# Performance work log

Hardware: AMD Instinct MI355X
Metric: run time of the kernel (lower is better)

Reference implementation:

```python
import jax, jax.numpy as jnp
import numpy as np

A = 4096      # alleles
RPA = 20      # mean reads per allele
R = A * RPA   # total reads per data source
C = 12        # input channels (pileup features)
L = 32        # read window length
D = 32        # hidden feature dim
NOUT = 2


def setup_inputs() -> dict:
    key = jax.random.key(0)
    k = jax.random.split(key, 8)
    # ragged read counts per allele (alternating 16/24, mean 20, sums to R)
    counts0 = np.tile(np.array([16, 24], dtype=np.int64), A // 2)
    counts1 = np.tile(np.array([24, 16], dtype=np.int64), A // 2)
    return {
        "tensors0": jax.random.normal(k[0], (R, C, L), dtype=jnp.float32),
        "tensors1": jax.random.normal(k[1], (R, C, L), dtype=jnp.float32),
        "W0": jax.random.normal(k[2], (D, C), dtype=jnp.float32) * 0.1,
        "b0": jnp.zeros((D,), dtype=jnp.float32),
        "W1": jax.random.normal(k[3], (D, C), dtype=jnp.float32) * 0.1,
        "b1": jnp.zeros((D,), dtype=jnp.float32),
        "W2": jax.random.normal(k[4], (NOUT, 2 * D), dtype=jnp.float32) * 0.1,
        "b2": jnp.zeros((NOUT,), dtype=jnp.float32),
        "numReadsPerAllele0": jnp.asarray(counts0),
        "numReadsPerAllele1": jnp.asarray(counts1),
        "numAllelesPerSite": jnp.full((A // 2,), 2, dtype=jnp.int64),
        "depthMultiplier0": jnp.asarray(counts0, dtype=jnp.float32),
        "depthMultiplier1": jnp.asarray(counts1, dtype=jnp.float32),
    }


def _frames(t, W, b):
    # pointwise read-feature extractor: [R,C,L] -> [R,D,L]
    return jax.nn.relu(jnp.einsum('rcl,dc->rdl', t, W) + b[None, :, None])


def reference(tensors0, tensors1, W0, b0, W1, b1, W2, b2,
              numReadsPerAllele0, numReadsPerAllele1,
              numAllelesPerSite, depthMultiplier0, depthMultiplier1):
    nA = numReadsPerAllele0.shape[0]
    nR = tensors0.shape[0]
    # segment ids replace torch.split + per-segment torch.sum (ragged segment-sum)
    seg0 = jnp.repeat(jnp.arange(nA), numReadsPerAllele0, total_repeat_length=nR)
    seg1 = jnp.repeat(jnp.arange(nA), numReadsPerAllele1, total_repeat_length=nR)

    frames0 = _frames(tensors0, W0, b0)  # [R,D,L]
    frames1 = _frames(tensors1, W1, b1)

    red0 = jax.ops.segment_sum(frames0, seg0, num_segments=nA)  # [A,D,L]
    red1 = jax.ops.segment_sum(frames1, seg1, num_segments=nA)

    # depth normalization (normalize() in the original)
    red0 = red0 / depthMultiplier0[:, None, None]
    red1 = red1 / depthMultiplier1[:, None, None]

    reduced = jnp.concatenate((red0, red1), axis=1)  # [A, 2D, L]

    # network2 (GraphSearcher): site-specific head modeled as pool + linear
    pooled = jnp.mean(reduced, axis=2)               # [A, 2D]
    return pooled @ W2.T + b2                        # [A, NOUT]
```

## Files before the change

### kernel.cpp

```cpp
#include <hip/hip_runtime.h>

#define A_ALLELES 4096
#define CCH 12
#define LW 32
#define DH 32
#define RDF (CCH * LW)

typedef __attribute__((ext_vector_type(8)))  short bf16x8;
typedef __attribute__((ext_vector_type(16))) float f32x16;

__device__ inline unsigned pk2(float fa, float fb) {
    const unsigned a = __float_as_uint(fa), b = __float_as_uint(fb);
    return ((a + 0x8000u) >> 16) | ((b + 0x8000u) & 0xffff0000u);
}

__global__ __launch_bounds__(256) void scan_kernel(
    const int* __restrict__ c0, const int* __restrict__ c1,
    int* __restrict__ o0, int* __restrict__ o1)
{
    const int* c = (blockIdx.x == 0) ? c0 : c1;
    int*       o = (blockIdx.x == 0) ? o0 : o1;

    __shared__ int part[256];
    const int tid  = threadIdx.x;
    const int base = tid * 16;

    int loc[16];
    int s = 0;
#pragma unroll
    for (int i = 0; i < 16; ++i) { loc[i] = c[base + i]; s += loc[i]; }
    part[tid] = s;
    __syncthreads();

    for (int st = 1; st < 256; st <<= 1) {
        int v = (tid >= st) ? part[tid - st] : 0;
        __syncthreads();
        part[tid] += v;
        __syncthreads();
    }

    int excl = (tid == 0) ? 0 : part[tid - 1];
#pragma unroll
    for (int i = 0; i < 16; ++i) { o[base + i] = excl; excl += loc[i]; }
}

__global__ __launch_bounds__(256, 4) void main_kernel(
    const float* __restrict__ t0, const float* __restrict__ t1,
    const float* __restrict__ W0, const float* __restrict__ b0,
    const float* __restrict__ W1, const float* __restrict__ b1,
    const float* __restrict__ W2, const float* __restrict__ b2,
    const int*  __restrict__ cnt0, const int* __restrict__ cnt1,
    const float* __restrict__ dm0, const float* __restrict__ dm1,
    const int*  __restrict__ offs0, const int* __restrict__ offs1,
    float* __restrict__ out)
{
    __shared__ float sW2[2 * 2 * DH];
    __shared__ float sB2[2];

    const int tid = threadIdx.x;
    if (tid < 2 * 2 * DH) sW2[tid] = W2[tid];
    if (tid < 2) sB2[tid] = b2[tid];
    __syncthreads();

    const int w    = tid >> 6;
    const int lane = tid & 63;
    const int src  = blockIdx.x >> 10;
    const int a    = ((blockIdx.x & 1023) << 2) | w;

    const float* __restrict__ tens = src ? t1 : t0;
    const int*   __restrict__ cnt  = src ? cnt1 : cnt0;
    const int*   __restrict__ offs = src ? offs1 : offs0;
    const float* __restrict__ dm   = src ? dm1 : dm0;
    const float* __restrict__ gW   = src ? W1 : W0;
    const float* __restrict__ gB   = src ? b1 : b0;

    const int l = lane & 31;
    const int h = lane >> 5;

    union { bf16x8 v; unsigned u[4]; } Af;
#pragma unroll
    for (int p = 0; p < 4; ++p) {
        const int c0 = h * 8 + 2 * p, c1 = c0 + 1;
        const float f0 = (c0 < CCH) ? gW[l * CCH + c0] : 0.f;
        const float f1 = (c1 < CCH) ? gW[l * CCH + c1] : 0.f;
        Af.u[p] = pk2(f0, f1);
    }
    f32x16 cb;
#pragma unroll
    for (int reg = 0; reg < 16; ++reg)
        cb[reg] = gB[(reg & 3) + 8 * (reg >> 2) + 4 * h];

    const int n     = cnt[a];
    const int start = offs[a];
    const float* rb  = tens + (size_t)start * RDF;
    const float* pLo = rb + l + h * 256;
    const float* pHi = rb + l + (h ? 256 : 128);

    float acc[16];
#pragma unroll
    for (int r = 0; r < 16; ++r) acc[r] = 0.f;

#define LOADR(B, i) do {                                              \
        const float* _pL = pLo + (size_t)(i) * RDF;                   \
        const float* _pH = pHi + (size_t)(i) * RDF;                   \
        B[0] = _pL[0];  B[1] = _pL[32]; B[2] = _pL[64]; B[3] = _pL[96]; \
        B[4] = _pH[0];  B[5] = _pH[32]; B[6] = _pH[64]; B[7] = _pH[96]; } while (0)

#define CONSUME(B) do {                                               \
        union { bf16x8 v; unsigned u[4]; } Bf;                        \
        Bf.u[0] = pk2(B[0], B[1]); Bf.u[1] = pk2(B[2], B[3]);         \
        Bf.u[2] = pk2(B[4], B[5]); Bf.u[3] = pk2(B[6], B[7]);         \
        const f32x16 Dv = __builtin_amdgcn_mfma_f32_32x32x16_bf16(    \
            Af.v, Bf.v, cb, 0, 0, 0);                                 \
        _Pragma("unroll")                                             \
        for (int r_ = 0; r_ < 16; ++r_) acc[r_] += fmaxf(Dv[r_], 0.f); } while (0)

    const int nf = n & ~3;
    if (nf >= 4) {
        float B0[8], B1[8], B2[8], B3[8];
        LOADR(B0, 0); LOADR(B1, 1); LOADR(B2, 2); LOADR(B3, 3);

        for (int g = 0; g + 8 <= nf; g += 4) {
            CONSUME(B0); LOADR(B0, g + 4);
            CONSUME(B1); LOADR(B1, g + 5);
            CONSUME(B2); LOADR(B2, g + 6);
            CONSUME(B3); LOADR(B3, g + 7);
        }
        CONSUME(B0); CONSUME(B1); CONSUME(B2); CONSUME(B3);
    }
    for (int i = nf; i < n; ++i) {
        float BT[8];
        LOADR(BT, i);
        CONSUME(BT);
    }
#undef LOADR
#undef CONSUME

#pragma unroll
    for (int r = 0; r < 16; ++r) {
#pragma unroll
        for (int mm = 1; mm < 32; mm <<= 1)
            acc[r] += __shfl_xor(acc[r], mm, 64);
    }

    const float scale = 1.f / (32.f * dm[a]);
    float c0s = 0.f, c1s = 0.f;
#pragma unroll
    for (int r = 0; r < 16; ++r) {
        const int d = (r & 3) + 8 * (r >> 2) + 4 * h;
        const float pv = acc[r] * scale;
        c0s = fmaf(pv, sW2[0 * 2 * DH + src * DH + d], c0s);
        c1s = fmaf(pv, sW2[1 * 2 * DH + src * DH + d], c1s);
    }
    c0s += __shfl_xor(c0s, 32, 64);
    c1s += __shfl_xor(c1s, 32, 64);

    if (lane == 0) {
        if (src == 0) { c0s += sB2[0]; c1s += sB2[1]; }
        atomicAdd(&out[a * 2 + 0], c0s);
        atomicAdd(&out[a * 2 + 1], c1s);
    }
}

extern "C" void kernel_launch(void* const* d_in, const int* in_sizes, int n_in,
                              void* d_out, int out_size, void* d_ws, size_t ws_size,
                              hipStream_t stream) {
    const float* t0  = (const float*)d_in[0];
    const float* t1  = (const float*)d_in[1];
    const float* W0  = (const float*)d_in[2];
    const float* b0  = (const float*)d_in[3];
    const float* W1  = (const float*)d_in[4];
    const float* b1  = (const float*)d_in[5];
    const float* W2  = (const float*)d_in[6];
    const float* b2  = (const float*)d_in[7];
    const int*  cnt0 = (const int*)d_in[8];
    const int*  cnt1 = (const int*)d_in[9];
    const float* dm0 = (const float*)d_in[11];
    const float* dm1 = (const float*)d_in[12];

    int* offs0 = (int*)d_ws;
    int* offs1 = offs0 + A_ALLELES;

    hipMemsetAsync(d_out, 0, (size_t)out_size * sizeof(float), stream);
    scan_kernel<<<2, 256, 0, stream>>>(cnt0, cnt1, offs0, offs1);

    main_kernel<<<2048, 256, 0, stream>>>(
        t0, t1, W0, b0, W1, b1, W2, b2,
        cnt0, cnt1, dm0, dm1, offs0, offs1, (float*)d_out);
}
```

Before: 316.8 us.

## Load reads as float2 and redistribute operands via lane shuffles

Replaces the eight strided scalar loads per lane with three 8-byte float2 loads per read, then rebuilds the MFMA B-operand layout using xor-1 and xor-32 lane shuffles. Each lane now holds fewer loads while every 384-float read is still fully covered. The prefetch depth drops from four reads in flight to two. The cost is extra shuffle and select instructions in the inner loop and less memory-level parallelism.

```diff
diff --git a/kernel.cpp b/kernel.cpp
--- a/kernel.cpp
+++ b/kernel.cpp
@@ -92,49 +92,67 @@
 
     const int n     = cnt[a];
     const int start = offs[a];
-    const float* rb  = tens + (size_t)start * RDF;
-    const float* pLo = rb + l + h * 256;
-    const float* pHi = rb + l + (h ? 256 : 128);
+    const float* rb = tens + (size_t)start * RDF;
+
+    const int e    = lane & 1;
+    const int jj   = (lane >> 1) & 15;
+    const int half = lane >> 5;
+    const int q0 = 2 * ((half * 8 + e)     * 16 + jj);
+    const int q1 = 2 * ((half * 8 + 2 + e) * 16 + jj);
+    const int q2 = 2 * ((4 + half * 2 + e) * 16 + jj);
 
     float acc[16];
 #pragma unroll
     for (int r = 0; r < 16; ++r) acc[r] = 0.f;
 
-#define LOADR(B, i) do {                                              \
-        const float* _pL = pLo + (size_t)(i) * RDF;                   \
-        const float* _pH = pHi + (size_t)(i) * RDF;                   \
-        B[0] = _pL[0];  B[1] = _pL[32]; B[2] = _pL[64]; B[3] = _pL[96]; \
-        B[4] = _pH[0];  B[5] = _pH[32]; B[6] = _pH[64]; B[7] = _pH[96]; } while (0)
-
-#define CONSUME(B) do {                                               \
+#define LOADF2(A0, A1, A2, i) do {                                    \
+        const float* _p = rb + (size_t)(i) * RDF;                     \
+        A0 = *reinterpret_cast<const float2*>(_p + q0);               \
+        A1 = *reinterpret_cast<const float2*>(_p + q1);               \
+        A2 = *reinterpret_cast<const float2*>(_p + q2); } while (0)
+
+#define CONSUMEF2(A0, A1, A2) do {                                    \
+        const float p0x = __shfl_xor(A0.x, 1, 64);                    \
+        const float p0y = __shfl_xor(A0.y, 1, 64);                    \
+        const float p1x = __shfl_xor(A1.x, 1, 64);                    \
+        const float p1y = __shfl_xor(A1.y, 1, 64);                    \
+        const float p2x = __shfl_xor(A2.x, 1, 64);                    \
+        const float p2y = __shfl_xor(A2.y, 1, 64);                    \
+        const float c0v = e ? p0y : A0.x;     \
+        const float c1v = e ? A0.y : p0x;    \
+        const float c2v = e ? p1y : A1.x;    \
+        const float c3v = e ? A1.y : p1x;    \
+        const float vA  = e ? p2y : A2.x;    \
+        const float vB  = e ? A2.y : p2x;    \
+        const float vC  = __shfl_xor(vA, 32, 64);      \
+        const float vD  = __shfl_xor(vB, 32, 64);      \
         union { bf16x8 v; unsigned u[4]; } Bf;                        \
-        Bf.u[0] = pk2(B[0], B[1]); Bf.u[1] = pk2(B[2], B[3]);         \
-        Bf.u[2] = pk2(B[4], B[5]); Bf.u[3] = pk2(B[6], B[7]);         \
+        Bf.u[0] = pk2(c0v, c1v); Bf.u[1] = pk2(c2v, c3v);             \
+        Bf.u[2] = pk2(vA, vB);   Bf.u[3] = pk2(vC, vD);               \
         const f32x16 Dv = __builtin_amdgcn_mfma_f32_32x32x16_bf16(    \
             Af.v, Bf.v, cb, 0, 0, 0);                                 \
         _Pragma("unroll")                                             \
         for (int r_ = 0; r_ < 16; ++r_) acc[r_] += fmaxf(Dv[r_], 0.f); } while (0)
 
-    const int nf = n & ~3;
-    if (nf >= 4) {
-        float B0[8], B1[8], B2[8], B3[8];
-        LOADR(B0, 0); LOADR(B1, 1); LOADR(B2, 2); LOADR(B3, 3);
-
-        for (int g = 0; g + 8 <= nf; g += 4) {
-            CONSUME(B0); LOADR(B0, g + 4);
-            CONSUME(B1); LOADR(B1, g + 5);
-            CONSUME(B2); LOADR(B2, g + 6);
-            CONSUME(B3); LOADR(B3, g + 7);
+    const int n2 = n & ~1;
+    if (n2 >= 2) {
+        float2 Ra0, Ra1, Ra2, Rb0, Rb1, Rb2;
+        LOADF2(Ra0, Ra1, Ra2, 0);
+        LOADF2(Rb0, Rb1, Rb2, 1);
+        for (int i = 0; i + 4 <= n2; i += 2) {
+            CONSUMEF2(Ra0, Ra1, Ra2); LOADF2(Ra0, Ra1, Ra2, i + 2);
+            CONSUMEF2(Rb0, Rb1, Rb2); LOADF2(Rb0, Rb1, Rb2, i + 3);
         }
-        CONSUME(B0); CONSUME(B1); CONSUME(B2); CONSUME(B3);
-    }
-    for (int i = nf; i < n; ++i) {
-        float BT[8];
-        LOADR(BT, i);
-        CONSUME(BT);
-    }
-#undef LOADR
-#undef CONSUME
+        CONSUMEF2(Ra0, Ra1, Ra2);
+        CONSUMEF2(Rb0, Rb1, Rb2);
+    }
+    for (int i = n2; i < n; ++i) {
+        float2 T0, T1, T2;
+        LOADF2(T0, T1, T2, i);
+        CONSUMEF2(T0, T1, T2);
+    }
+#undef LOADF2
+#undef CONSUMEF2
 
 #pragma unroll
     for (int r = 0; r < 16; ++r) {
```

After: 298.2 us. 5.8% less time.
